# Kernel tuning notes

Measured on AMD Instinct MI355X. Metric: run time of the kernel, lower is better.

## Reference

```python
import jax, jax.numpy as jnp
import numpy as np
import math

DIM = 1024
NUM_HEADS = 16
HEAD_DIM = DIM // NUM_HEADS
B, S = 2, 2048

def setup_inputs() -> dict:
    key = jax.random.key(0)
    ks = jax.random.split(key, 9)
    sc = 0.02
    return {
        "x": jax.random.normal(ks[0], (B, S, DIM), jnp.float32),
        "Wq": jax.random.normal(ks[1], (DIM, DIM), jnp.float32) * sc,
        "bq": jax.random.normal(ks[2], (DIM,), jnp.float32) * sc,
        "Wk": jax.random.normal(ks[3], (DIM, DIM), jnp.float32) * sc,
        "bk": jax.random.normal(ks[4], (DIM,), jnp.float32) * sc,
        "Wv": jax.random.normal(ks[5], (DIM, DIM), jnp.float32) * sc,
        "bv": jax.random.normal(ks[6], (DIM,), jnp.float32) * sc,
        "Wo": jax.random.normal(ks[7], (DIM, DIM), jnp.float32) * sc,
        "bo": jax.random.normal(ks[8], (DIM,), jnp.float32) * sc,
    }

def reference(x, Wq, bq, Wk, bk, Wv, bv, Wo, bo):
    b, s, d = x.shape
    h, hd = NUM_HEADS, HEAD_DIM
    # qkv projections: [B,S,D] -> [B,H,S,hd]
    def split_heads(t):
        return t.reshape(b, s, h, hd).transpose(0, 2, 1, 3)
    q = split_heads(x @ Wq + bq)
    k = split_heads(x @ Wk + bk)
    v = split_heads(x @ Wv + bv)
    # scores [B,H,S,S], scale, causal mask via where(-10000), softmax
    scores = jnp.einsum('bhqd,bhkd->bhqk', q, k) / math.sqrt(hd)
    causal = jnp.tril(jnp.ones((s, s), dtype=bool))  # [S,S]
    scores = jnp.where(causal[None, None], scores, jnp.asarray(-10000.0, scores.dtype))
    probs = jax.nn.softmax(scores, axis=-1)
    ctx = jnp.einsum('bhqk,bhkd->bhqd', probs, v)
    ctx = ctx.transpose(0, 2, 1, 3).reshape(b, s, d)
    return ctx @ Wo + bo
```

## Files before the change

kernel.cpp:

```cpp
#include <hip/hip_runtime.h>
#include <hip/hip_bf16.h>

#define DIM 1024
#define NUM_HEADS 16
#define HEAD_DIM 64
#define BATCH 2
#define SEQ 2048
#define M_ROWS (BATCH * SEQ)

typedef short bh8 __attribute__((ext_vector_type(8)));
typedef float f32x4 __attribute__((ext_vector_type(4)));
typedef float f32x16 __attribute__((ext_vector_type(16)));

#define SCALE_Q 0.18033688011116016f

#define MFMA16(a, b, c) __builtin_amdgcn_mfma_f32_16x16x32_bf16(a, b, c, 0, 0, 0)
#define MFMA32(a, b, c) __builtin_amdgcn_mfma_f32_32x32x16_bf16(a, b, c, 0, 0, 0)

#if __has_builtin(__builtin_amdgcn_exp2f)
#define EXP2F(x) __builtin_amdgcn_exp2f(x)
#else
#define EXP2F(x) exp2f(x)
#endif

__device__ __forceinline__ ushort f2bf(float f) {
    union { float f; unsigned u; } v; v.f = f;
    unsigned u = v.u;
    unsigned r = (u + 0x7FFFu + ((u >> 16) & 1u)) >> 16;
    return (ushort)r;
}

__device__ __forceinline__ unsigned cvt_pk_bf16(float lo, float hi) {
    unsigned r;
    asm("v_cvt_pk_bf16_f32 %0, %1, %2" : "=v"(r) : "v"(lo), "v"(hi));
    return r;
}

__device__ __forceinline__ void plane_swap(unsigned a, unsigned b,
                                           unsigned& o0, unsigned& o1, int h) {
#if __has_builtin(__builtin_amdgcn_permlane32_swap)
    (void)h;
    auto pr = __builtin_amdgcn_permlane32_swap(a, b, false, false);
    unsigned o[2]; __builtin_memcpy(o, &pr, 8);
    o0 = o[0]; o1 = o[1];
#else
    unsigned sa = (unsigned)__shfl_xor((int)a, 32);
    unsigned sb = (unsigned)__shfl_xor((int)b, 32);
    o0 = h ? sb : a;
    o1 = h ? b : sa;
#endif
}

__device__ __forceinline__ void async_cp16(const ushort* g, ushort* l) {
    __builtin_amdgcn_global_load_lds(
        (const __attribute__((address_space(1))) void*)(uintptr_t)g,
        (__attribute__((address_space(3))) void*)(uint32_t)(uintptr_t)l,
        16, 0, 0);
}

__global__ __launch_bounds__(256) void prep_inputs(
    const float* __restrict__ W0, const float* __restrict__ W1,
    const float* __restrict__ W2, const float* __restrict__ W3,
    const float* __restrict__ x,
    ushort* __restrict__ T0, ushort* __restrict__ T1,
    ushort* __restrict__ T2, ushort* __restrict__ T3,
    ushort* __restrict__ xb)
{
    const int z = blockIdx.z;
    const int t = threadIdx.x;
    if (z == 4) {
        int base = (blockIdx.y * 32 + blockIdx.x) * 1024 + t;
        const float4* in4 = (const float4*)x;
        ushort4* out4 = (ushort4*)xb;
        #pragma unroll
        for (int i = 0; i < 4; ++i) {
            float4 v = in4[base + i * 256];
            ushort4 o;
            o.x = f2bf(v.x); o.y = f2bf(v.y); o.z = f2bf(v.z); o.w = f2bf(v.w);
            out4[base + i * 256] = o;
        }
        return;
    }
    __shared__ float tile[32][33];
    const float* W = (z == 0) ? W0 : (z == 1) ? W1 : (z == 2) ? W2 : W3;
    ushort* Wt = (z == 0) ? T0 : (z == 1) ? T1 : (z == 2) ? T2 : T3;
    const int tx = t & 31, ty = t >> 5;
    const int k0 = blockIdx.y * 32, n0 = blockIdx.x * 32;
    #pragma unroll
    for (int i = 0; i < 4; ++i)
        tile[ty + 8 * i][tx] = W[(size_t)(k0 + ty + 8 * i) * DIM + n0 + tx];
    __syncthreads();
    #pragma unroll
    for (int i = 0; i < 4; ++i)
        Wt[(size_t)(n0 + ty + 8 * i) * DIM + k0 + tx] = f2bf(tile[tx][ty + 8 * i]);
}

#define GTM 128
#define GTN 64
#define GBK 64

__device__ __forceinline__ void gemm_core(
    const ushort* __restrict__ A, const ushort* __restrict__ Bt,
    ushort* smem, int m0, int n0, int t, f32x4 acc[4][2])
{
    ushort* As = smem;
    ushort* Bs = smem + 8192;
    const int lane = t & 63, wave = t >> 6;
    const int col = lane & 15, quad = lane >> 4;
    const int wm = (wave & 1) * 64, wn = (wave >> 1) * 32;

    for (int k0 = 0; k0 < DIM; k0 += GBK) {
        __syncthreads();
        #pragma unroll
        for (int j = 0; j < 4; ++j) {
            int C = wave * 256 + j * 64 + lane;
            int row = C >> 3;
            int lch = (C & 7) ^ (row & 7);
            async_cp16(&A[(size_t)(m0 + row) * DIM + k0 + lch * 8],
                       &As[(wave * 256 + j * 64) * 8]);
        }
        #pragma unroll
        for (int j = 0; j < 2; ++j) {
            int C = wave * 128 + j * 64 + lane;
            int row = C >> 3;
            int lch = (C & 7) ^ (row & 7);
            async_cp16(&Bt[(size_t)(n0 + row) * DIM + k0 + lch * 8],
                       &Bs[(wave * 128 + j * 64) * 8]);
        }
        __syncthreads();
        #pragma unroll
        for (int kk = 0; kk < 2; ++kk) {
            bh8 af[4], bfr[2];
            #pragma unroll
            for (int mi = 0; mi < 4; ++mi) {
                int row = wm + mi * 16 + col;
                af[mi] = *(const bh8*)&As[row * 64 + (((kk * 4 + quad) ^ (row & 7)) * 8)];
            }
            #pragma unroll
            for (int ni = 0; ni < 2; ++ni) {
                int row = wn + ni * 16 + col;
                bfr[ni] = *(const bh8*)&Bs[row * 64 + (((kk * 4 + quad) ^ (row & 7)) * 8)];
            }
            #pragma unroll
            for (int mi = 0; mi < 4; ++mi)
                #pragma unroll
                for (int ni = 0; ni < 2; ++ni)
                    acc[mi][ni] = MFMA16(af[mi], bfr[ni], acc[mi][ni]);
        }
    }
}

__global__ __launch_bounds__(256) void gemm_qkv(
    const ushort* __restrict__ A,
    const ushort* __restrict__ WqT, const ushort* __restrict__ WkT,
    const ushort* __restrict__ WvT,
    const float* __restrict__ bq, const float* __restrict__ bk,
    const float* __restrict__ bv,
    ushort* __restrict__ qo, ushort* __restrict__ ko_, ushort* __restrict__ vo)
{
    __shared__ ushort smem[12288];
    const int z = blockIdx.z;
    const ushort* Bt = (z == 0) ? WqT : (z == 1) ? WkT : WvT;
    const float* bias = (z == 0) ? bq : (z == 1) ? bk : bv;
    ushort* outp = (z == 0) ? qo : (z == 1) ? ko_ : vo;

    const int t = threadIdx.x;
    const int lane = t & 63, wave = t >> 6;
    const int col = lane & 15, quad = lane >> 4;
    const int m0 = blockIdx.y * GTM, n0 = blockIdx.x * GTN;
    const int wm = (wave & 1) * 64, wn = (wave >> 1) * 32;
    f32x4 acc[4][2] = {};

    gemm_core(A, Bt, smem, m0, n0, t, acc);

    const int b = m0 >> 11, s0 = m0 & (SEQ - 1);
    const int h = n0 >> 6;

    if (z < 2) {
        const float scl = (z == 0) ? SCALE_Q : 1.f;
        __syncthreads();
        ushort* LT = smem;
        #pragma unroll
        for (int mi = 0; mi < 4; ++mi)
            #pragma unroll
            for (int ni = 0; ni < 2; ++ni) {
                int dl = wn + ni * 16 + col;
                float bvv = bias[n0 + dl];
                #pragma unroll
                for (int r = 0; r < 4; ++r) {
                    int ml = wm + mi * 16 + quad * 4 + r;
                    LT[ml * 72 + dl] = f2bf((acc[mi][ni][r] + bvv) * scl);
                }
            }
        __syncthreads();
        ushort* Cp = outp + (((size_t)(b * NUM_HEADS + h) * SEQ + s0) << 6);
        #pragma unroll
        for (int i = 0; i < 4; ++i) {
            int c = i * 256 + t;
            int row = c >> 3, ko = (c & 7) * 8;
            *(uint4*)&Cp[row * 64 + ko] = *(const uint4*)&LT[row * 72 + ko];
        }
    } else {
        __syncthreads();
        ushort* LT = smem;
        #pragma unroll
        for (int mi = 0; mi < 4; ++mi)
            #pragma unroll
            for (int ni = 0; ni < 2; ++ni) {
                int nl = wn + ni * 16 + col;
                float bvv = bias[n0 + nl];
                #pragma unroll
                for (int r = 0; r < 4; ++r) {
                    int ml = wm + mi * 16 + quad * 4 + r;
                    LT[nl * 136 + ml] = f2bf(acc[mi][ni][r] + bvv);
                }
            }
        __syncthreads();
        ushort* Cp = outp + (((size_t)(b * NUM_HEADS + h) * HEAD_DIM) << 11);
        #pragma unroll
        for (int i = 0; i < 4; ++i) {
            int c = i * 256 + t;
            int row = c >> 4, mo = (c & 15) * 8;
            *(uint4*)&Cp[((size_t)row << 11) + s0 + mo] = *(const uint4*)&LT[row * 136 + mo];
        }
    }
}

__global__ __launch_bounds__(256) void gemm_out(
    const ushort* __restrict__ A, const ushort* __restrict__ Bt,
    const float* __restrict__ bias, float* __restrict__ C)
{
    __shared__ ushort smem[12288];
    const int t = threadIdx.x;
    const int lane = t & 63, wave = t >> 6;
    const int col = lane & 15, quad = lane >> 4;
    const int m0 = blockIdx.y * GTM, n0 = blockIdx.x * GTN;
    const int wm = (wave & 1) * 64, wn = (wave >> 1) * 32;
    f32x4 acc[4][2] = {};

    gemm_core(A, Bt, smem, m0, n0, t, acc);

    #pragma unroll
    for (int mi = 0; mi < 4; ++mi)
        #pragma unroll
        for (int ni = 0; ni < 2; ++ni) {
            int n = n0 + wn + ni * 16 + col;
            float bvv = bias[n];
            #pragma unroll
            for (int r = 0; r < 4; ++r) {
                int m = m0 + wm + mi * 16 + quad * 4 + r;
                C[(size_t)m * DIM + n] = acc[mi][ni][r] + bvv;
            }
        }
}

__global__ __launch_bounds__(256, 4) void attn_mfma(
    const ushort* __restrict__ Qg, const ushort* __restrict__ Kg,
    const ushort* __restrict__ Vtg, ushort* __restrict__ ctx)
{
    __shared__ char smem[17408];
    float* OA   = (float*)smem;
    float* OB   = (float*)(smem + 8448);
    float* lbuf = (float*)(smem + 16896);

    const int t = threadIdx.x;
    const int lane = t & 63, wave = t >> 6;
    const int q32 = lane & 31, h = lane >> 5;
    const int bh = blockIdx.x & 31;
    const int qt = 63 - (blockIdx.x >> 5);
    const int b = bh >> 4, hd = bh & 15;
    const int q0 = qt << 5;
    const int kw0 = wave * 32;
    const ushort* Kp = Kg + ((size_t)bh << 17);
    const ushort* Vp = Vtg + ((size_t)bh << 17);
    const ushort* Qp = Qg + ((size_t)bh << 17);

    bh8 qf[4];
    #pragma unroll
    for (int kc = 0; kc < 4; ++kc)
        qf[kc] = *(const bh8*)&Qp[((size_t)(q0 + q32) << 6) + kc * 16 + h * 8];

    f32x16 O[2] = {};
    float l = 0.f;
    const int nIter = (q0 + 159) >> 7;

    bh8 kf[4], vf[2][2];
    #pragma unroll
    for (int kc = 0; kc < 4; ++kc)
        kf[kc] = *(const bh8*)&Kp[((size_t)(kw0 + q32) << 6) + kc * 16 + h * 8];
    #pragma unroll
    for (int dti = 0; dti < 2; ++dti)
        #pragma unroll
        for (int kc = 0; kc < 2; ++kc)
            vf[dti][kc] = *(const bh8*)&Vp[((size_t)(dti * 32 + q32) << 11)
                                           + kw0 + kc * 16 + h * 8];

    #pragma unroll 1
    for (int it = 0; it < nIter; ++it) {
        const int kb = it << 7;
        if (kb + kw0 > q0 + 31) break;

        f32x16 St = {};
        #pragma unroll
        for (int kc = 0; kc < 4; ++kc)
            St = MFMA32(kf[kc], qf[kc], St);

        const int kb2 = kb + 128;
        if (it + 1 < nIter) {
            #pragma unroll
            for (int kc = 0; kc < 4; ++kc)
                kf[kc] = *(const bh8*)&Kp[((size_t)(kb2 + kw0 + q32) << 6)
                                          + kc * 16 + h * 8];
        }

        if (kb + kw0 + 31 > q0) {
            int q_abs = q0 + q32;
            #pragma unroll
            for (int r = 0; r < 16; ++r) {
                int key_abs = kb + kw0 + (r & 3) + ((r >> 2) << 3) + 4 * h;
                if (key_abs > q_abs) St[r] = -1e30f;
            }
        }

        float p[16];
        #pragma unroll
        for (int r = 0; r < 16; ++r) p[r] = EXP2F(St[r]);
        float t0 = (p[0] + p[1]) + (p[2] + p[3]);
        float t1 = (p[4] + p[5]) + (p[6] + p[7]);
        float t2 = (p[8] + p[9]) + (p[10] + p[11]);
        float t3 = (p[12] + p[13]) + (p[14] + p[15]);
        l += (t0 + t1) + (t2 + t3);

        unsigned w[8];
        #pragma unroll
        for (int m = 0; m < 8; ++m) w[m] = cvt_pk_bf16(p[2 * m], p[2 * m + 1]);
        unsigned j0, j1, j2, j3, j4, j5, j6, j7;
        plane_swap(w[0], w[2], j0, j2, h);
        plane_swap(w[1], w[3], j1, j3, h);
        plane_swap(w[4], w[6], j4, j6, h);
        plane_swap(w[5], w[7], j5, j7, h);
        union { unsigned u[4]; bh8 v; } pu0, pu1;
        pu0.u[0] = j0; pu0.u[1] = j1; pu0.u[2] = j2; pu0.u[3] = j3;
        pu1.u[0] = j4; pu1.u[1] = j5; pu1.u[2] = j6; pu1.u[3] = j7;

        O[0] = MFMA32(vf[0][0], pu0.v, O[0]);
        O[1] = MFMA32(vf[1][0], pu0.v, O[1]);
        O[0] = MFMA32(vf[0][1], pu1.v, O[0]);
        O[1] = MFMA32(vf[1][1], pu1.v, O[1]);

        if (it + 1 < nIter) {
            #pragma unroll
            for (int dti = 0; dti < 2; ++dti)
                #pragma unroll
                for (int kc = 0; kc < 2; ++kc)
                    vf[dti][kc] = *(const bh8*)&Vp[((size_t)(dti * 32 + q32) << 11)
                                                   + kb2 + kw0 + kc * 16 + h * 8];
        }
    }

    l += __shfl_xor(l, 32);
    if (h == 0) lbuf[wave * 32 + q32] = l;
    __syncthreads();

    if (wave == 1 || wave == 3) {
        float* dst = (wave == 1) ? OA : OB;
        #pragma unroll
        for (int dti = 0; dti < 2; ++dti)
            #pragma unroll
            for (int r = 0; r < 16; ++r) {
                int d_l = dti * 32 + (r & 3) + ((r >> 2) << 3) + 4 * h;
                dst[d_l * 33 + q32] = O[dti][r];
            }
    }
    __syncthreads();
    if (wave == 0 || wave == 2) {
        float* src = (wave == 0) ? OA : OB;
        #pragma unroll
        for (int dti = 0; dti < 2; ++dti)
            #pragma unroll
            for (int r = 0; r < 16; ++r) {
                int d_l = dti * 32 + (r & 3) + ((r >> 2) << 3) + 4 * h;
                O[dti][r] += src[d_l * 33 + q32];
            }
    }
    __syncthreads();
    if (wave == 2) {
        #pragma unroll
        for (int dti = 0; dti < 2; ++dti)
            #pragma unroll
            for (int r = 0; r < 16; ++r) {
                int d_l = dti * 32 + (r & 3) + ((r >> 2) << 3) + 4 * h;
                OA[d_l * 33 + q32] = O[dti][r];
            }
    }
    __syncthreads();
    if (wave == 0) {
        float tot = lbuf[q32] + lbuf[32 + q32] + lbuf[64 + q32] + lbuf[96 + q32];
        float inv = 1.f / tot;
        ushort* Oq = (ushort*)(smem + 8448);
        #pragma unroll
        for (int dti = 0; dti < 2; ++dti)
            #pragma unroll
            for (int rg = 0; rg < 4; ++rg) {
                int d0 = dti * 32 + rg * 8 + 4 * h;
                float s0 = (O[dti][rg * 4 + 0] + OA[(d0 + 0) * 33 + q32]) * inv;
                float s1 = (O[dti][rg * 4 + 1] + OA[(d0 + 1) * 33 + q32]) * inv;
                float s2 = (O[dti][rg * 4 + 2] + OA[(d0 + 2) * 33 + q32]) * inv;
                float s3 = (O[dti][rg * 4 + 3] + OA[(d0 + 3) * 33 + q32]) * inv;
                uint2 pk; pk.x = cvt_pk_bf16(s0, s1); pk.y = cvt_pk_bf16(s2, s3);
                *(uint2*)&Oq[q32 * 72 + d0] = pk;
            }
        #pragma unroll
        for (int i = 0; i < 4; ++i) {
            int c = i * 64 + lane;
            int row = c >> 3, ko = (c & 7) * 8;
            *(uint4*)&ctx[((size_t)(b * SEQ) + q0 + row) * DIM + (hd << 6) + ko] =
                *(const uint4*)&Oq[row * 72 + ko];
        }
    }
}

extern "C" void kernel_launch(void* const* d_in, const int* in_sizes, int n_in,
                              void* d_out, int out_size, void* d_ws, size_t ws_size,
                              hipStream_t stream) {
    const float* x  = (const float*)d_in[0];
    const float* Wq = (const float*)d_in[1];
    const float* bq = (const float*)d_in[2];
    const float* Wk = (const float*)d_in[3];
    const float* bk = (const float*)d_in[4];
    const float* Wv = (const float*)d_in[5];
    const float* bv = (const float*)d_in[6];
    const float* Wo = (const float*)d_in[7];
    const float* bo = (const float*)d_in[8];
    float* out = (float*)d_out;

    ushort* x_bf   = (ushort*)d_ws;
    ushort* wq_t   = x_bf + 4194304;
    ushort* wk_t   = wq_t + 1048576;
    ushort* wv_t   = wk_t + 1048576;
    ushort* wo_t   = wv_t + 1048576;
    ushort* q_ws   = wo_t + 1048576;
    ushort* k_ws   = q_ws + 4194304;
    ushort* vt_ws  = k_ws + 4194304;
    ushort* ctx_ws = vt_ws + 4194304;

    dim3 pgrid(32, 32, 5);
    prep_inputs<<<pgrid, 256, 0, stream>>>(Wq, Wk, Wv, Wo, x,
                                           wq_t, wk_t, wv_t, wo_t, x_bf);

    dim3 qkv_grid(DIM / GTN, M_ROWS / GTM, 3);
    gemm_qkv<<<qkv_grid, 256, 0, stream>>>(x_bf, wq_t, wk_t, wv_t,
                                           bq, bk, bv, q_ws, k_ws, vt_ws);

    attn_mfma<<<2048, 256, 0, stream>>>(q_ws, k_ws, vt_ws, ctx_ws);

    dim3 ogrid(DIM / GTN, M_ROWS / GTM);
    gemm_out<<<ogrid, 256, 0, stream>>>(ctx_ws, wo_t, bo, out);
}
```

Measured before the change: 209.2 us.

## Process two key subtiles per wave in attention and swizzle GEMM block order

The attention kernel now has each wave handle two 32-key subtiles per iteration, a 256-key step instead of 128, to raise per-wave ILP. It double-buffers K/V fragments for both subtiles, wraps the MFMA groups in s_setprio, and lowers the launch-bounds occupancy hint from 4 to 2 blocks per CU. Both GEMM kernels remap their block indices with a grouped swizzle to improve L2 reuse of A and weight tiles. The extra register pressure and lower occupancy hint may cut latency hiding, and the second subtile is skipped near the causal diagonal, so some waves sit idle there.

```diff
diff --git a/kernel.cpp b/kernel.cpp
--- a/kernel.cpp
+++ b/kernel.cpp
@@ -159,7 +159,10 @@
     ushort* __restrict__ qo, ushort* __restrict__ ko_, ushort* __restrict__ vo)
 {
     __shared__ ushort smem[12288];
-    const int z = blockIdx.z;
+    const int lin = blockIdx.x + 16 * blockIdx.y + 512 * blockIdx.z;
+    const int swz = (lin & 7) * 192 + (lin >> 3);
+    const int bx = swz & 15, by = (swz >> 4) & 31, z = swz >> 9;
+
     const ushort* Bt = (z == 0) ? WqT : (z == 1) ? WkT : WvT;
     const float* bias = (z == 0) ? bq : (z == 1) ? bk : bv;
     ushort* outp = (z == 0) ? qo : (z == 1) ? ko_ : vo;
@@ -167,7 +170,7 @@
     const int t = threadIdx.x;
     const int lane = t & 63, wave = t >> 6;
     const int col = lane & 15, quad = lane >> 4;
-    const int m0 = blockIdx.y * GTM, n0 = blockIdx.x * GTN;
+    const int m0 = by * GTM, n0 = bx * GTN;
     const int wm = (wave & 1) * 64, wn = (wave >> 1) * 32;
     f32x4 acc[4][2] = {};
 
@@ -231,10 +234,14 @@
     const float* __restrict__ bias, float* __restrict__ C)
 {
     __shared__ ushort smem[12288];
+    const int lin = blockIdx.x + 16 * blockIdx.y;
+    const int swz = (lin & 7) * 64 + (lin >> 3);
+    const int bx = swz & 15, by = swz >> 4;
+
     const int t = threadIdx.x;
     const int lane = t & 63, wave = t >> 6;
     const int col = lane & 15, quad = lane >> 4;
-    const int m0 = blockIdx.y * GTM, n0 = blockIdx.x * GTN;
+    const int m0 = by * GTM, n0 = bx * GTN;
     const int wm = (wave & 1) * 64, wn = (wave >> 1) * 32;
     f32x4 acc[4][2] = {};
 
@@ -254,7 +261,7 @@
         }
 }
 
-__global__ __launch_bounds__(256, 4) void attn_mfma(
+__global__ __launch_bounds__(256, 2) void attn_mfma(
     const ushort* __restrict__ Qg, const ushort* __restrict__ Kg,
     const ushort* __restrict__ Vtg, ushort* __restrict__ ctx)
 {
@@ -270,7 +277,7 @@
     const int qt = 63 - (blockIdx.x >> 5);
     const int b = bh >> 4, hd = bh & 15;
     const int q0 = qt << 5;
-    const int kw0 = wave * 32;
+    const int kwA = wave * 64, kwB = wave * 64 + 32;
     const ushort* Kp = Kg + ((size_t)bh << 17);
     const ushort* Vp = Vtg + ((size_t)bh << 17);
     const ushort* Qp = Qg + ((size_t)bh << 17);
@@ -282,79 +289,134 @@
 
     f32x16 O[2] = {};
     float l = 0.f;
-    const int nIter = (q0 + 159) >> 7;
-
-    bh8 kf[4], vf[2][2];
+    const int nIter = (q0 + 287) >> 8;
+
+    bh8 kfa[4], kfb[4], vfa[2][2], vfb[2][2];
     #pragma unroll
-    for (int kc = 0; kc < 4; ++kc)
-        kf[kc] = *(const bh8*)&Kp[((size_t)(kw0 + q32) << 6) + kc * 16 + h * 8];
+    for (int kc = 0; kc < 4; ++kc) {
+        kfa[kc] = *(const bh8*)&Kp[((size_t)(kwA + q32) << 6) + kc * 16 + h * 8];
+        kfb[kc] = *(const bh8*)&Kp[((size_t)(kwB + q32) << 6) + kc * 16 + h * 8];
+    }
     #pragma unroll
     for (int dti = 0; dti < 2; ++dti)
         #pragma unroll
-        for (int kc = 0; kc < 2; ++kc)
-            vf[dti][kc] = *(const bh8*)&Vp[((size_t)(dti * 32 + q32) << 11)
-                                           + kw0 + kc * 16 + h * 8];
+        for (int kc = 0; kc < 2; ++kc) {
+            vfa[dti][kc] = *(const bh8*)&Vp[((size_t)(dti * 32 + q32) << 11)
+                                            + kwA + kc * 16 + h * 8];
+            vfb[dti][kc] = *(const bh8*)&Vp[((size_t)(dti * 32 + q32) << 11)
+                                            + kwB + kc * 16 + h * 8];
+        }
 
     #pragma unroll 1
     for (int it = 0; it < nIter; ++it) {
-        const int kb = it << 7;
-        if (kb + kw0 > q0 + 31) break;
-
-        f32x16 St = {};
+        const int kb = it << 8;
+        if (kb + kwA > q0 + 31) break;
+        const bool bAct = (kb + kwB <= q0 + 31);
+
+        f32x16 StA = {}, StB = {};
+        __builtin_amdgcn_s_setprio(1);
         #pragma unroll
         for (int kc = 0; kc < 4; ++kc)
-            St = MFMA32(kf[kc], qf[kc], St);
-
-        const int kb2 = kb + 128;
+            StA = MFMA32(kfa[kc], qf[kc], StA);
+        if (bAct) {
+            #pragma unroll
+            for (int kc = 0; kc < 4; ++kc)
+                StB = MFMA32(kfb[kc], qf[kc], StB);
+        }
+        __builtin_amdgcn_s_setprio(0);
+
+        const int kb2 = kb + 256;
         if (it + 1 < nIter) {
             #pragma unroll
-            for (int kc = 0; kc < 4; ++kc)
-                kf[kc] = *(const bh8*)&Kp[((size_t)(kb2 + kw0 + q32) << 6)
-                                          + kc * 16 + h * 8];
-        }
-
-        if (kb + kw0 + 31 > q0) {
-            int q_abs = q0 + q32;
+            for (int kc = 0; kc < 4; ++kc) {
+                kfa[kc] = *(const bh8*)&Kp[((size_t)(kb2 + kwA + q32) << 6)
+                                           + kc * 16 + h * 8];
+                kfb[kc] = *(const bh8*)&Kp[((size_t)(kb2 + kwB + q32) << 6)
+                                           + kc * 16 + h * 8];
+            }
+        }
+
+        const int q_abs = q0 + q32;
+        if (kb + kwA + 31 > q0) {
             #pragma unroll
             for (int r = 0; r < 16; ++r) {
-                int key_abs = kb + kw0 + (r & 3) + ((r >> 2) << 3) + 4 * h;
-                if (key_abs > q_abs) St[r] = -1e30f;
-            }
-        }
-
-        float p[16];
-        #pragma unroll
-        for (int r = 0; r < 16; ++r) p[r] = EXP2F(St[r]);
-        float t0 = (p[0] + p[1]) + (p[2] + p[3]);
-        float t1 = (p[4] + p[5]) + (p[6] + p[7]);
-        float t2 = (p[8] + p[9]) + (p[10] + p[11]);
-        float t3 = (p[12] + p[13]) + (p[14] + p[15]);
-        l += (t0 + t1) + (t2 + t3);
-
-        unsigned w[8];
-        #pragma unroll
-        for (int m = 0; m < 8; ++m) w[m] = cvt_pk_bf16(p[2 * m], p[2 * m + 1]);
-        unsigned j0, j1, j2, j3, j4, j5, j6, j7;
-        plane_swap(w[0], w[2], j0, j2, h);
-        plane_swap(w[1], w[3], j1, j3, h);
-        plane_swap(w[4], w[6], j4, j6, h);
-        plane_swap(w[5], w[7], j5, j7, h);
-        union { unsigned u[4]; bh8 v; } pu0, pu1;
-        pu0.u[0] = j0; pu0.u[1] = j1; pu0.u[2] = j2; pu0.u[3] = j3;
-        pu1.u[0] = j4; pu1.u[1] = j5; pu1.u[2] = j6; pu1.u[3] = j7;
-
-        O[0] = MFMA32(vf[0][0], pu0.v, O[0]);
-        O[1] = MFMA32(vf[1][0], pu0.v, O[1]);
-        O[0] = MFMA32(vf[0][1], pu1.v, O[0]);
-        O[1] = MFMA32(vf[1][1], pu1.v, O[1]);
+                int key_abs = kb + kwA + (r & 3) + ((r >> 2) << 3) + 4 * h;
+                if (key_abs > q_abs) StA[r] = -1e30f;
+            }
+        }
+        if (bAct && kb + kwB + 31 > q0) {
+            #pragma unroll
+            for (int r = 0; r < 16; ++r) {
+                int key_abs = kb + kwB + (r & 3) + ((r >> 2) << 3) + 4 * h;
+                if (key_abs > q_abs) StB[r] = -1e30f;
+            }
+        }
+
+        union { unsigned u[4]; bh8 v; } puA0, puA1, puB0, puB1;
+        {
+            float p[16];
+            #pragma unroll
+            for (int r = 0; r < 16; ++r) p[r] = EXP2F(StA[r]);
+            float t0 = (p[0] + p[1]) + (p[2] + p[3]);
+            float t1 = (p[4] + p[5]) + (p[6] + p[7]);
+            float t2 = (p[8] + p[9]) + (p[10] + p[11]);
+            float t3 = (p[12] + p[13]) + (p[14] + p[15]);
+            l += (t0 + t1) + (t2 + t3);
+            unsigned w[8];
+            #pragma unroll
+            for (int m = 0; m < 8; ++m) w[m] = cvt_pk_bf16(p[2 * m], p[2 * m + 1]);
+            unsigned j0, j1, j2, j3, j4, j5, j6, j7;
+            plane_swap(w[0], w[2], j0, j2, h);
+            plane_swap(w[1], w[3], j1, j3, h);
+            plane_swap(w[4], w[6], j4, j6, h);
+            plane_swap(w[5], w[7], j5, j7, h);
+            puA0.u[0] = j0; puA0.u[1] = j1; puA0.u[2] = j2; puA0.u[3] = j3;
+            puA1.u[0] = j4; puA1.u[1] = j5; puA1.u[2] = j6; puA1.u[3] = j7;
+        }
+        if (bAct) {
+            float p[16];
+            #pragma unroll
+            for (int r = 0; r < 16; ++r) p[r] = EXP2F(StB[r]);
+            float t0 = (p[0] + p[1]) + (p[2] + p[3]);
+            float t1 = (p[4] + p[5]) + (p[6] + p[7]);
+            float t2 = (p[8] + p[9]) + (p[10] + p[11]);
+            float t3 = (p[12] + p[13]) + (p[14] + p[15]);
+            l += (t0 + t1) + (t2 + t3);
+            unsigned w[8];
+            #pragma unroll
+            for (int m = 0; m < 8; ++m) w[m] = cvt_pk_bf16(p[2 * m], p[2 * m + 1]);
+            unsigned j0, j1, j2, j3, j4, j5, j6, j7;
+            plane_swap(w[0], w[2], j0, j2, h);
+            plane_swap(w[1], w[3], j1, j3, h);
+            plane_swap(w[4], w[6], j4, j6, h);
+            plane_swap(w[5], w[7], j5, j7, h);
+            puB0.u[0] = j0; puB0.u[1] = j1; puB0.u[2] = j2; puB0.u[3] = j3;
+            puB1.u[0] = j4; puB1.u[1] = j5; puB1.u[2] = j6; puB1.u[3] = j7;
+        }
+
+        __builtin_amdgcn_s_setprio(1);
+        O[0] = MFMA32(vfa[0][0], puA0.v, O[0]);
+        O[1] = MFMA32(vfa[1][0], puA0.v, O[1]);
+        O[0] = MFMA32(vfa[0][1], puA1.v, O[0]);
+        O[1] = MFMA32(vfa[1][1], puA1.v, O[1]);
+        if (bAct) {
+            O[0] = MFMA32(vfb[0][0], puB0.v, O[0]);
+            O[1] = MFMA32(vfb[1][0], puB0.v, O[1]);
+            O[0] = MFMA32(vfb[0][1], puB1.v, O[0]);
+            O[1] = MFMA32(vfb[1][1], puB1.v, O[1]);
+        }
+        __builtin_amdgcn_s_setprio(0);
 
         if (it + 1 < nIter) {
             #pragma unroll
             for (int dti = 0; dti < 2; ++dti)
                 #pragma unroll
-                for (int kc = 0; kc < 2; ++kc)
-                    vf[dti][kc] = *(const bh8*)&Vp[((size_t)(dti * 32 + q32) << 11)
-                                                   + kb2 + kw0 + kc * 16 + h * 8];
+                for (int kc = 0; kc < 2; ++kc) {
+                    vfa[dti][kc] = *(const bh8*)&Vp[((size_t)(dti * 32 + q32) << 11)
+                                                    + kb2 + kwA + kc * 16 + h * 8];
+                    vfb[dti][kc] = *(const bh8*)&Vp[((size_t)(dti * 32 + q32) << 11)
+                                                    + kb2 + kwB + kc * 16 + h * 8];
+                }
         }
     }
 
```

Result: no change. 209.3 us (+0.0%).
